# Optimization experiments

Hardware: AMD Instinct MI355X
Metric: run time of the kernel (lower is better)

The kernel has to match this reference:

```python
import jax, jax.numpy as jnp
import numpy as np

NUM_NODES = 2048
NUM_REL = 8
HIDDEN = 256


def setup_inputs() -> dict:
    key = jax.random.key(0)
    k1, k2, k3 = jax.random.split(key, 3)
    X = jax.random.normal(k1, (NUM_NODES, HIDDEN, NUM_REL), dtype=jnp.float32)
    A = jax.random.uniform(k2, (NUM_NODES, NUM_NODES, NUM_REL), dtype=jnp.float32)
    # nn.init.normal_(std=0.01)
    weight = 0.01 * jax.random.normal(k3, (HIDDEN, HIDDEN, NUM_REL), dtype=jnp.float32)
    return {"X": X, "A": A, "weight": weight}


def _tensor_product(A, B):
    # Faithful to the original: FFT along last (relation) dim, take REAL part of
    # both transformed operands, per-slice matmul, then real part of ifft.
    Af = jnp.real(jnp.fft.fft(A, axis=-1))  # (n1, n2, k)
    Bf = jnp.real(jnp.fft.fft(B, axis=-1))  # (n2, n4, k)
    C = jnp.einsum('nmk,mhk->nhk', Af, Bf)  # batched real matmul over slices k
    return jnp.real(jnp.fft.ifft(C, axis=-1)).astype(A.dtype)


def reference(X, A, weight):
    res = _tensor_product(A, X)          # (num_nodes, hidden, num_rel)
    res = _tensor_product(res, weight)   # (num_nodes, hidden, num_rel)
    return res
```

## Files before the change

### kernel.cpp

```cpp
#include <hip/hip_runtime.h>


typedef __bf16 bf16_t;
typedef __bf16 bf16x8 __attribute__((ext_vector_type(8)));
typedef float f32x4 __attribute__((ext_vector_type(4)));

#define R2C 0.70710678118654752f

__device__ __forceinline__ void fwd5(const float x[8], float F[5]) {
  float s04 = x[0] + x[4], d04 = x[0] - x[4];
  float s26 = x[2] + x[6];
  float s15 = x[1] + x[5], s37 = x[3] + x[7];
  float t = (x[1] + x[7]) - (x[3] + x[5]);
  float e = s04 + s26, o = s15 + s37;
  F[0] = e + o;
  F[1] = d04 + R2C * t;
  F[2] = s04 - s26;
  F[3] = d04 - R2C * t;
  F[4] = e - o;
}

__global__ __launch_bounds__(256) void k_xf(const float* __restrict__ X,
                                            bf16_t* __restrict__ Xft) {
  int m = blockIdx.x * 256 + threadIdx.x;
  int h = blockIdx.y;
  const float4* p = (const float4*)(X + ((size_t)m * 256 + h) * 8);
  float4 a = p[0], b = p[1];
  float x[8] = {a.x, a.y, a.z, a.w, b.x, b.y, b.z, b.w};
  float F[5];
  fwd5(x, F);
  size_t base = (size_t)h * 2048 + m;
#pragma unroll
  for (int j = 0; j < 5; j++) Xft[(size_t)j * 524288 + base] = (bf16_t)F[j];
}

__global__ __launch_bounds__(256) void k_wf(const float* __restrict__ W,
                                            bf16_t* __restrict__ Wft) {
  int hp = threadIdx.x;
  int h = blockIdx.y;
  const float4* p = (const float4*)(W + ((size_t)hp * 256 + h) * 8);
  float4 a = p[0], b = p[1];
  float x[8] = {a.x, a.y, a.z, a.w, b.x, b.y, b.z, b.w};
  float F[5];
  fwd5(x, F);
  const float sc[5] = {0.125f, 0.25f, 0.25f, 0.25f, 0.125f};
  size_t base = (size_t)h * 256 + hp;
#pragma unroll
  for (int j = 0; j < 5; j++) Wft[(size_t)j * 65536 + base] = (bf16_t)(F[j] * sc[j]);
}

__global__ __launch_bounds__(256) void k_af(const float* __restrict__ A,
                                            bf16_t* __restrict__ Af) {
  size_t idx = (size_t)blockIdx.x * 256 + threadIdx.x;
  const float4* p = (const float4*)(A + idx * 8);
  float4 a = p[0], b = p[1];
  float x[8] = {a.x, a.y, a.z, a.w, b.x, b.y, b.z, b.w};
  float F[5];
  fwd5(x, F);
#pragma unroll
  for (int j = 0; j < 5; j++) Af[(size_t)j * 4194304 + idx] = (bf16_t)F[j];
}

template <typename OutT>
__global__ __launch_bounds__(256) void gemm5(const bf16_t* __restrict__ A,
                                             const bf16_t* __restrict__ B,
                                             OutT* __restrict__ C, int K,
                                             size_t ap, size_t bp, size_t cp) {
  constexpr int BK = 64;
  __shared__ bf16_t As[128 * BK];
  __shared__ bf16_t Bs[128 * BK];
  const int j = blockIdx.z;
  const bf16_t* Aj = A + (size_t)j * ap;
  const bf16_t* Bj = B + (size_t)j * bp;
  OutT* Cj = C + (size_t)j * cp;
  const int n0 = blockIdx.x * 128, h0 = blockIdx.y * 128;
  const int tid = threadIdx.x;
  const int wv = tid >> 6, ln = tid & 63;
  const int quad = ln >> 4, l16 = ln & 15;
  const int wn = (wv & 1) * 64, wh = (wv >> 1) * 64;
  f32x4 acc[4][4] = {};

  for (int kk = 0; kk < K; kk += BK) {
    __syncthreads();
#pragma unroll
    for (int s = 0; s < 4; s++) {
      int slot = tid + s * 256;
      int row = slot >> 3;
      int c16 = slot & 7;
      int dst = row * 64 + (((c16) ^ (row & 7)) << 3);
      size_t goff = (size_t)kk + c16 * 8;
      uint4 va = *(const uint4*)(Aj + (size_t)(n0 + row) * K + goff);
      uint4 vb = *(const uint4*)(Bj + (size_t)(h0 + row) * K + goff);
      *(uint4*)(As + dst) = va;
      *(uint4*)(Bs + dst) = vb;
    }
    __syncthreads();
#pragma unroll
    for (int kh = 0; kh < 2; kh++) {
      bf16x8 af[4], bfr[4];
      int c16 = kh * 4 + quad;
#pragma unroll
      for (int i = 0; i < 4; i++) {
        int ra = wn + i * 16 + l16;
        int rb = wh + i * 16 + l16;
        af[i] = *(const bf16x8*)(As + ra * 64 + ((c16 ^ (ra & 7)) << 3));
        bfr[i] = *(const bf16x8*)(Bs + rb * 64 + ((c16 ^ (rb & 7)) << 3));
      }
#pragma unroll
      for (int i = 0; i < 4; i++)
#pragma unroll
        for (int t = 0; t < 4; t++)
          acc[i][t] = __builtin_amdgcn_mfma_f32_16x16x32_bf16(af[i], bfr[t],
                                                              acc[i][t], 0, 0, 0);
    }
  }
#pragma unroll
  for (int i = 0; i < 4; i++) {
#pragma unroll
    for (int t = 0; t < 4; t++) {
      int hc = h0 + wh + t * 16 + l16;
#pragma unroll
      for (int rg = 0; rg < 4; rg++) {
        int nr = n0 + wn + i * 16 + quad * 4 + rg;
        Cj[(size_t)nr * 256 + hc] = (OutT)acc[i][t][rg];
      }
    }
  }
}

__global__ __launch_bounds__(256) void k_combine(const float* __restrict__ C2,
                                                 float* __restrict__ out) {
  size_t idx = (size_t)blockIdx.x * 256 + threadIdx.x;
  float c0 = C2[idx];
  float c1 = C2[524288 + idx];
  float c2 = C2[2 * 524288 + idx];
  float c3 = C2[3 * 524288 + idx];
  float c4 = C2[4 * 524288 + idx];
  float o0 = c0 + c1 + c2 + c3 + c4;
  float o4 = c0 - c1 + c2 - c3 + c4;
  float o2 = c0 - c2 + c4;
  float rt = R2C * (c1 - c3);
  float o1 = c0 + rt - c4;
  float o3 = c0 - rt - c4;
  float4* op = (float4*)(out + idx * 8);
  op[0] = make_float4(o0, o1, o2, o3);
  op[1] = make_float4(o4, o3, o2, o1);
}

extern "C" void kernel_launch(void* const* d_in, const int* in_sizes, int n_in,
                              void* d_out, int out_size, void* d_ws, size_t ws_size,
                              hipStream_t stream) {
  const float* X = (const float*)d_in[0];
  const float* A = (const float*)d_in[1];
  const float* W = (const float*)d_in[2];
  float* out = (float*)d_out;
  char* ws = (char*)d_ws;

  bf16_t* Af  = (bf16_t*)(ws);
  bf16_t* Xft = (bf16_t*)(ws + 41943040);
  bf16_t* Wft = (bf16_t*)(ws + 47185920);
  bf16_t* C1  = (bf16_t*)(ws + 47841280);
  float*  C2  = (float*) (ws + 53084160);

  k_xf<<<dim3(8, 256), 256, 0, stream>>>(X, Xft);
  k_wf<<<dim3(1, 256), 256, 0, stream>>>(W, Wft);
  k_af<<<dim3(16384), 256, 0, stream>>>(A, Af);
  gemm5<bf16_t><<<dim3(16, 2, 5), 256, 0, stream>>>(Af, Xft, C1, 2048,
                                                    (size_t)4194304, (size_t)524288,
                                                    (size_t)524288);
  gemm5<float><<<dim3(16, 2, 5), 256, 0, stream>>>(C1, Wft, C2, 256,
                                                   (size_t)524288, (size_t)65536,
                                                   (size_t)524288);
  k_combine<<<dim3(2048), 256, 0, stream>>>(C2, out);
}
```

Measured before the change: 271.3 us.

## Split-K the big GEMM, prefetch global tiles, and merge preprocessing kernels

Result: slower. 312.6 us (+15.2%).

```diff
diff --git a/kernel.cpp b/kernel.cpp
--- a/kernel.cpp
+++ b/kernel.cpp
@@ -2,6 +2,7 @@
 
 
 typedef __bf16 bf16_t;
+typedef __bf16 bf16x2 __attribute__((ext_vector_type(2)));
 typedef __bf16 bf16x8 __attribute__((ext_vector_type(8)));
 typedef float f32x4 __attribute__((ext_vector_type(4)));
 
@@ -20,81 +21,116 @@
   F[4] = e - o;
 }
 
-__global__ __launch_bounds__(256) void k_xf(const float* __restrict__ X,
-                                            bf16_t* __restrict__ Xft) {
-  int m = blockIdx.x * 256 + threadIdx.x;
-  int h = blockIdx.y;
-  const float4* p = (const float4*)(X + ((size_t)m * 256 + h) * 8);
-  float4 a = p[0], b = p[1];
-  float x[8] = {a.x, a.y, a.z, a.w, b.x, b.y, b.z, b.w};
-  float F[5];
-  fwd5(x, F);
-  size_t base = (size_t)h * 2048 + m;
-#pragma unroll
-  for (int j = 0; j < 5; j++) Xft[(size_t)j * 524288 + base] = (bf16_t)F[j];
-}
-
-__global__ __launch_bounds__(256) void k_wf(const float* __restrict__ W,
-                                            bf16_t* __restrict__ Wft) {
-  int hp = threadIdx.x;
-  int h = blockIdx.y;
-  const float4* p = (const float4*)(W + ((size_t)hp * 256 + h) * 8);
-  float4 a = p[0], b = p[1];
-  float x[8] = {a.x, a.y, a.z, a.w, b.x, b.y, b.z, b.w};
-  float F[5];
-  fwd5(x, F);
-  const float sc[5] = {0.125f, 0.25f, 0.25f, 0.25f, 0.125f};
-  size_t base = (size_t)h * 256 + hp;
-#pragma unroll
-  for (int j = 0; j < 5; j++) Wft[(size_t)j * 65536 + base] = (bf16_t)(F[j] * sc[j]);
-}
-
-__global__ __launch_bounds__(256) void k_af(const float* __restrict__ A,
-                                            bf16_t* __restrict__ Af) {
-  size_t idx = (size_t)blockIdx.x * 256 + threadIdx.x;
-  const float4* p = (const float4*)(A + idx * 8);
-  float4 a = p[0], b = p[1];
-  float x[8] = {a.x, a.y, a.z, a.w, b.x, b.y, b.z, b.w};
-  float F[5];
-  fwd5(x, F);
-#pragma unroll
-  for (int j = 0; j < 5; j++) Af[(size_t)j * 4194304 + idx] = (bf16_t)F[j];
-}
-
-template <typename OutT>
-__global__ __launch_bounds__(256) void gemm5(const bf16_t* __restrict__ A,
-                                             const bf16_t* __restrict__ B,
-                                             OutT* __restrict__ C, int K,
-                                             size_t ap, size_t bp, size_t cp) {
-  constexpr int BK = 64;
-  __shared__ bf16_t As[128 * BK];
-  __shared__ bf16_t Bs[128 * BK];
-  const int j = blockIdx.z;
+__global__ __launch_bounds__(256) void k_pre(const float* __restrict__ X,
+                                             const float* __restrict__ A,
+                                             const float* __restrict__ W,
+                                             bf16_t* __restrict__ Xft,
+                                             bf16_t* __restrict__ Af,
+                                             bf16_t* __restrict__ Wft) {
+  int b = blockIdx.x;
+  if (b < 8192) {
+    size_t t = (size_t)b * 256 + threadIdx.x;
+    size_t idx = t * 2;
+    const float4* p = (const float4*)(A + idx * 8);
+    float4 q0 = p[0], q1 = p[1], q2 = p[2], q3 = p[3];
+    float x0[8] = {q0.x, q0.y, q0.z, q0.w, q1.x, q1.y, q1.z, q1.w};
+    float x1[8] = {q2.x, q2.y, q2.z, q2.w, q3.x, q3.y, q3.z, q3.w};
+    float F0[5], F1[5];
+    fwd5(x0, F0);
+    fwd5(x1, F1);
+#pragma unroll
+    for (int j = 0; j < 5; j++) {
+      bf16x2 v = {(bf16_t)F0[j], (bf16_t)F1[j]};
+      *(bf16x2*)(Af + (size_t)j * 4194304 + idx) = v;
+    }
+  } else if (b < 9216) {
+    size_t t = (size_t)(b - 8192) * 256 + threadIdx.x;
+    int h = (int)(t >> 10);
+    int m = (int)(t & 1023) * 2;
+    const float4* p0 = (const float4*)(X + ((size_t)m * 256 + h) * 8);
+    const float4* p1 = (const float4*)(X + ((size_t)(m + 1) * 256 + h) * 8);
+    float4 a0 = p0[0], b0 = p0[1], a1 = p1[0], b1 = p1[1];
+    float x0[8] = {a0.x, a0.y, a0.z, a0.w, b0.x, b0.y, b0.z, b0.w};
+    float x1[8] = {a1.x, a1.y, a1.z, a1.w, b1.x, b1.y, b1.z, b1.w};
+    float F0[5], F1[5];
+    fwd5(x0, F0);
+    fwd5(x1, F1);
+    size_t base = (size_t)h * 2048 + m;
+#pragma unroll
+    for (int j = 0; j < 5; j++) {
+      bf16x2 v = {(bf16_t)F0[j], (bf16_t)F1[j]};
+      *(bf16x2*)(Xft + (size_t)j * 524288 + base) = v;
+    }
+  } else {
+    int h = b - 9216;
+    int hp = threadIdx.x;
+    const float4* p = (const float4*)(W + ((size_t)hp * 256 + h) * 8);
+    float4 a = p[0], bb = p[1];
+    float x[8] = {a.x, a.y, a.z, a.w, bb.x, bb.y, bb.z, bb.w};
+    float F[5];
+    fwd5(x, F);
+    const float sc[5] = {0.125f, 0.25f, 0.25f, 0.25f, 0.125f};
+    size_t base = (size_t)h * 256 + hp;
+#pragma unroll
+    for (int j = 0; j < 5; j++)
+      Wft[(size_t)j * 65536 + base] = (bf16_t)(F[j] * sc[j]);
+  }
+}
+
+__global__ __launch_bounds__(256) void gemm_k(const bf16_t* __restrict__ A,
+                                              const bf16_t* __restrict__ B,
+                                              float* __restrict__ C, int K,
+                                              int KS, size_t ap, size_t bp,
+                                              size_t cp) {
+  __shared__ bf16_t As[128 * 64];
+  __shared__ bf16_t Bs[128 * 64];
+  const int z = blockIdx.z, j = z % 5, s = z / 5;
   const bf16_t* Aj = A + (size_t)j * ap;
   const bf16_t* Bj = B + (size_t)j * bp;
-  OutT* Cj = C + (size_t)j * cp;
+  float* Cj = C + (size_t)z * cp;
   const int n0 = blockIdx.x * 128, h0 = blockIdx.y * 128;
   const int tid = threadIdx.x;
   const int wv = tid >> 6, ln = tid & 63;
   const int quad = ln >> 4, l16 = ln & 15;
   const int wn = (wv & 1) * 64, wh = (wv >> 1) * 64;
+  const int k0 = s * KS, k1 = k0 + KS;
+
+  const bf16_t* pa[4];
+  const bf16_t* pb[4];
+  int dsts[4];
+#pragma unroll
+  for (int t = 0; t < 4; t++) {
+    int slot = tid + t * 256;
+    int row = slot >> 3, c16 = slot & 7;
+    dsts[t] = row * 64 + ((c16 ^ (row & 7)) << 3);
+    pa[t] = Aj + (size_t)(n0 + row) * K + k0 + c16 * 8;
+    pb[t] = Bj + (size_t)(h0 + row) * K + k0 + c16 * 8;
+  }
+  uint4 va[4], vb[4];
+#pragma unroll
+  for (int t = 0; t < 4; t++) {
+    va[t] = *(const uint4*)pa[t];
+    vb[t] = *(const uint4*)pb[t];
+  }
+
   f32x4 acc[4][4] = {};
-
-  for (int kk = 0; kk < K; kk += BK) {
+  for (int kk = k0; kk < k1; kk += 64) {
     __syncthreads();
 #pragma unroll
-    for (int s = 0; s < 4; s++) {
-      int slot = tid + s * 256;
-      int row = slot >> 3;
-      int c16 = slot & 7;
-      int dst = row * 64 + (((c16) ^ (row & 7)) << 3);
-      size_t goff = (size_t)kk + c16 * 8;
-      uint4 va = *(const uint4*)(Aj + (size_t)(n0 + row) * K + goff);
-      uint4 vb = *(const uint4*)(Bj + (size_t)(h0 + row) * K + goff);
-      *(uint4*)(As + dst) = va;
-      *(uint4*)(Bs + dst) = vb;
+    for (int t = 0; t < 4; t++) {
+      *(uint4*)(As + dsts[t]) = va[t];
+      *(uint4*)(Bs + dsts[t]) = vb[t];
     }
     __syncthreads();
+    if (kk + 64 < k1) {
+#pragma unroll
+      for (int t = 0; t < 4; t++) {
+        pa[t] += 64;
+        pb[t] += 64;
+        va[t] = *(const uint4*)pa[t];
+        vb[t] = *(const uint4*)pb[t];
+      }
+    }
 #pragma unroll
     for (int kh = 0; kh < 2; kh++) {
       bf16x8 af[4], bfr[4];
@@ -122,10 +158,22 @@
 #pragma unroll
       for (int rg = 0; rg < 4; rg++) {
         int nr = n0 + wn + i * 16 + quad * 4 + rg;
-        Cj[(size_t)nr * 256 + hc] = (OutT)acc[i][t][rg];
+        Cj[(size_t)nr * 256 + hc] = acc[i][t][rg];
       }
     }
   }
+}
+
+__global__ __launch_bounds__(256) void k_red(const float* __restrict__ C1p,
+                                             bf16_t* __restrict__ C1) {
+  size_t idx = ((size_t)blockIdx.x * 256 + threadIdx.x) * 2;
+  float2 a0 = *(const float2*)(C1p + idx);
+  float2 a1 = *(const float2*)(C1p + 2621440 + idx);
+  float2 a2 = *(const float2*)(C1p + 2 * 2621440 + idx);
+  float2 a3 = *(const float2*)(C1p + 3 * 2621440 + idx);
+  bf16x2 v = {(bf16_t)(a0.x + a1.x + a2.x + a3.x),
+              (bf16_t)(a0.y + a1.y + a2.y + a3.y)};
+  *(bf16x2*)(C1 + idx) = v;
 }
 
 __global__ __launch_bounds__(256) void k_combine(const float* __restrict__ C2,
@@ -159,17 +207,17 @@
   bf16_t* Af  = (bf16_t*)(ws);
   bf16_t* Xft = (bf16_t*)(ws + 41943040);
   bf16_t* Wft = (bf16_t*)(ws + 47185920);
-  bf16_t* C1  = (bf16_t*)(ws + 47841280);
-  float*  C2  = (float*) (ws + 53084160);
-
-  k_xf<<<dim3(8, 256), 256, 0, stream>>>(X, Xft);
-  k_wf<<<dim3(1, 256), 256, 0, stream>>>(W, Wft);
-  k_af<<<dim3(16384), 256, 0, stream>>>(A, Af);
-  gemm5<bf16_t><<<dim3(16, 2, 5), 256, 0, stream>>>(Af, Xft, C1, 2048,
-                                                    (size_t)4194304, (size_t)524288,
-                                                    (size_t)524288);
-  gemm5<float><<<dim3(16, 2, 5), 256, 0, stream>>>(C1, Wft, C2, 256,
-                                                   (size_t)524288, (size_t)65536,
-                                                   (size_t)524288);
+  float*  C1p = (float*) (ws + 47841280);
+  bf16_t* C1  = (bf16_t*)(ws + 89784320);
+  float*  C2  = (float*) (ws + 95027200);
+
+  k_pre<<<dim3(9472), 256, 0, stream>>>(X, A, W, Xft, Af, Wft);
+  gemm_k<<<dim3(16, 2, 20), 256, 0, stream>>>(Af, Xft, C1p, 2048, 512,
+                                              (size_t)4194304, (size_t)524288,
+                                              (size_t)524288);
+  k_red<<<dim3(5120), 256, 0, stream>>>(C1p, C1);
+  gemm_k<<<dim3(16, 2, 5), 256, 0, stream>>>(C1, Wft, C2, 256, 256,
+                                             (size_t)524288, (size_t)65536,
+                                             (size_t)524288);
   k_combine<<<dim3(2048), 256, 0, stream>>>(C2, out);
 }
```
